# Optimization experiments

Measured on AMD Instinct MI355X. Metric: run time of the kernel, lower is better.

Reference implementation:

```python
import jax, jax.numpy as jnp
import numpy as np

NF = 64      # feature channels of h
K = 3        # dynamic filter spatial size (padding=1 in source implies k=3)
FACTOR = 4   # pixel-unshuffle factor


def shuffle_down(x, f):
    # torch pixel_unshuffle: (B,C,H*f,W*f) -> (B,C*f*f,H,W)
    B, C, H, W = x.shape
    x = x.reshape(B, C, H // f, f, W // f, f)
    x = x.transpose(0, 1, 3, 5, 2, 4)
    return x.reshape(B, C * f * f, H // f, W // f)


def _patches3x3(x):
    # x: (B,C,H,W) -> (B,C,9,H,W): zero-padded 3x3 neighborhoods, row-major taps,
    # identical to the identity-filter grouped conv (im2col) in the source.
    H, W = x.shape[-2], x.shape[-1]
    xp = jnp.pad(x, ((0, 0), (0, 0), (1, 1), (1, 1)))
    shifts = [xp[:, :, dy:dy + H, dx:dx + W] for dy in range(K) for dx in range(K)]
    return jnp.stack(shifts, axis=2)


def setup_inputs() -> dict:
    key = jax.random.key(0)
    k1, k2, k3, k4 = jax.random.split(key, 4)
    B, H, W = 2, 256, 256
    h = jax.random.normal(k1, (B, NF, H, W), dtype=jnp.float32)
    i_t = jax.random.normal(k2, (B, 3, H * FACTOR, W * FACTOR), dtype=jnp.float32)
    conv_w = jax.random.normal(k3, (K * K, 3 * FACTOR ** 2, K, K), dtype=jnp.float32) * 0.05
    conv_b = jax.random.normal(k4, (K * K,), dtype=jnp.float32) * 0.05
    return {"h": h, "i_t": i_t, "conv_w": conv_w, "conv_b": conv_b}


def reference(h, i_t, conv_w, conv_b):
    # predict per-pixel 3x3 filters from the shuffled-down guidance frame
    x = shuffle_down(i_t, FACTOR)  # (B, 48, H, W)
    f = jax.lax.conv_general_dilated(
        x, conv_w, window_strides=(1, 1), padding=((1, 1), (1, 1)),
        dimension_numbers=("NCHW", "OIHW", "NCHW"))
    filters = jax.nn.relu(f + conv_b[None, :, None, None])  # (B, 9, H, W)

    # dynamic per-pixel conv: same 3x3 filter applied to every channel of h
    patches = _patches3x3(h)  # (B, nf, 9, H, W)
    out = jnp.einsum("bcfhw,bfhw->bchw", patches, filters)  # (B, nf, H, W)
    return out
```

## Files before the change

### kernel.cpp

```cpp
#include <hip/hip_runtime.h>

#define TILE 16
#define HSZ 256
#define WSZ 256
#define NFC 64
#define PLANE (HSZ * WSZ)

typedef __attribute__((ext_vector_type(8))) short short8;
typedef __attribute__((ext_vector_type(4))) float f32x4;

__device__ inline unsigned short f2bf(float f) {
    unsigned u = __builtin_bit_cast(unsigned, f);
    return (unsigned short)((u + 0x7fffu + ((u >> 16) & 1u)) >> 16);
}

__global__ void prep_wfrag(const float* __restrict__ wbuf,
                           unsigned short* __restrict__ wfragG)
{
    const int kb   = blockIdx.x;
    const int lane = threadIdx.x;
    const int l15  = lane & 15;
    const int kg   = lane >> 4;
    unsigned short v8[8];
#pragma unroll
    for (int j = 0; j < 8; ++j) {
        const int k = kb * 32 + kg * 8 + j;
        float w = 0.f;
        if (k < 432 && l15 < 9) {
            const int kk = k / 48;
            const int ic = k - kk * 48;
            w = wbuf[l15 * 432 + ic * 9 + kk];
        }
        v8[j] = f2bf(w);
    }
    unsigned short* p = wfragG + (size_t)kb * 512 + lane * 8;
    *(ushort4*)(p)     = ushort4{v8[0], v8[1], v8[2], v8[3]};
    *(ushort4*)(p + 4) = ushort4{v8[4], v8[5], v8[6], v8[7]};
}

__global__ __launch_bounds__(256) void filter_conv_mfma3(
    const float* __restrict__ i_t,
    const unsigned short* __restrict__ wfragG,
    const float* __restrict__ bias,
    float* __restrict__ fbuf, int Bn)
{
    __shared__ __align__(16) unsigned short xs[180 * 48];

    const int tid  = threadIdx.x;
    const int X0 = blockIdx.x * 16;
    const int Y0 = blockIdx.y * 8;
    const int b  = blockIdx.z;
    const int lane = tid & 63;
    const int l15  = tid & 15;
    const int kg   = (tid >> 4) & 3;
    const int wv   = tid >> 6;

    const float bv = (l15 < 9) ? bias[l15] : 0.f;
    const float* itb = i_t + (size_t)b * 3 * (PLANE * 16);

    {
        float4 lreg[9]; int sdst[9];
#pragma unroll
        for (int k = 0; k < 9; ++k) {
            const int v = tid + 256 * k;
            const int sp = v / 12, t = v - sp * 12;
            const int c3 = t >> 2, fy = t & 3;
            const int ly = sp / 18, lx = sp - ly * 18;
            const int Y = Y0 - 1 + ly, X = X0 - 1 + lx;
            float4 val = make_float4(0.f, 0.f, 0.f, 0.f);
            if (v < 2160 && (unsigned)Y < HSZ && (unsigned)X < WSZ)
                val = *(const float4*)(itb + ((size_t)c3 * 1024 + (4 * Y + fy)) * 1024 + 4 * X);
            lreg[k] = val;
            sdst[k] = (v < 2160) ? (sp * 48 + t * 4) : -1;
        }
#pragma unroll
        for (int k = 0; k < 9; ++k) {
            if (sdst[k] >= 0) {
                ushort4 u{f2bf(lreg[k].x), f2bf(lreg[k].y), f2bf(lreg[k].z), f2bf(lreg[k].w)};
                *(ushort4*)(xs + sdst[k]) = u;
            }
        }
    }

    short8 wf[14];
#pragma unroll
    for (int kb = 0; kb < 14; ++kb)
        wf[kb] = *(const short8*)(wfragG + (size_t)kb * 512 + lane * 8);

    __syncthreads();

    f32x4 acc0 = {0.f, 0.f, 0.f, 0.f}, acc1 = acc0;
#pragma unroll
    for (int kb = 0; kb < 14; ++kb) {
        const int k0 = kb * 32 + kg * 8;
        int off = 0;
        if (k0 < 432) {
            const int kk  = k0 / 48;
            const int ic0 = k0 - kk * 48;
            const int ky  = kk / 3;
            const int kx  = kk - 3 * ky;
            off = ((2 * wv + ky) * 18 + l15 + kx) * 48 + ic0;
        }
        short8 a0 = *(const short8*)(xs + off);
        short8 a1 = *(const short8*)(xs + off + 864);
        acc0 = __builtin_amdgcn_mfma_f32_16x16x32_bf16(a0, wf[kb], acc0, 0, 0, 0);
        acc1 = __builtin_amdgcn_mfma_f32_16x16x32_bf16(a1, wf[kb], acc1, 0, 0, 0);
    }

    __syncthreads();
    float* lf = (float*)xs;
    if (l15 < 9) {
#pragma unroll
        for (int t = 0; t < 2; ++t) {
            const int py = 2 * wv + t;
            f32x4 A = t ? acc1 : acc0;
#pragma unroll
            for (int r = 0; r < 4; ++r) {
                const int px = kg * 4 + r;
                lf[l15 * 128 + py * 16 + px] = fmaxf(A[r] + bv, 0.f);
            }
        }
    }
    __syncthreads();
    {
        const int v0 = tid;
        const int oc = v0 >> 5, rem = v0 & 31, py = rem >> 2, xf4 = rem & 3;
        *(float4*)(fbuf + ((size_t)oc * Bn + b) * PLANE + (size_t)(Y0 + py) * WSZ + X0 + xf4 * 4)
            = *(const float4*)(lf + oc * 128 + py * 16 + xf4 * 4);
        if (tid < 32) {
            const int v1 = tid + 256;
            const int oc1 = v1 >> 5, rem1 = v1 & 31, py1 = rem1 >> 2, xf41 = rem1 & 3;
            *(float4*)(fbuf + ((size_t)oc1 * Bn + b) * PLANE + (size_t)(Y0 + py1) * WSZ + X0 + xf41 * 4)
                = *(const float4*)(lf + oc1 * 128 + py1 * 16 + xf41 * 4);
        }
    }
}

__global__ __launch_bounds__(256, 4) void dyn_apply5(
    const float* __restrict__ hbuf,
    const float* __restrict__ fbuf,
    float* __restrict__ out, int Bn)
{
    __shared__ __align__(16) float hs[8 * 720];

    const int tid  = threadIdx.x;
    const int pq   = tid & 7;
    const int py   = (tid >> 3) & 15;
    const int c_lo = tid >> 7;
    const int cg = blockIdx.x & 7;
    const int X0 = (blockIdx.x >> 3) * 32;
    const int Y0 = blockIdx.y * TILE;
    const int b  = blockIdx.z;

    float4 flt4[9];
    {
        const size_t pix = (size_t)b * PLANE + (size_t)(Y0 + py) * WSZ + X0 + pq * 4;
#pragma unroll
        for (int oc = 0; oc < 9; ++oc)
            flt4[oc] = *(const float4*)(fbuf + (size_t)oc * Bn * PLANE + pix);
    }

    const float* hp = hbuf + ((size_t)b * NFC + cg * 8) * PLANE;
    {
        float4 rv[6]; int dst[6];
#pragma unroll
        for (int k = 0; k < 6; ++k) {
            const int v = tid + 256 * k;
            const int c = v / 180;
            const int r = v - c * 180;
            const int row = r / 10, xq = r - row * 10;
            const int Y  = Y0 - 1 + row;
            const int X4 = X0 - 4 + xq * 4;
            float4 val = make_float4(0.f, 0.f, 0.f, 0.f);
            if (v < 1440 && (unsigned)Y < HSZ && (unsigned)X4 < WSZ)
                val = *(const float4*)(hp + (size_t)c * PLANE + (size_t)Y * WSZ + X4);
            rv[k] = val;
            dst[k] = (v < 1440) ? (c * 720 + row * 40 + xq * 4) : -1;
        }
#pragma unroll
        for (int k = 0; k < 6; ++k)
            if (dst[k] >= 0) *(float4*)(hs + dst[k]) = rv[k];
    }
    __syncthreads();

    float a[4][4];
#pragma unroll
    for (int cc = 0; cc < 4; ++cc)
#pragma unroll
        for (int j = 0; j < 4; ++j) a[cc][j] = 0.f;

#pragma unroll
    for (int cc = 0; cc < 4; ++cc) {
        const float* pl = hs + (c_lo + 2 * cc) * 720;
#pragma unroll
        for (int ky = 0; ky < 3; ++ky) {
            const float* rp = pl + (py + ky) * 40 + pq * 4;
            float4 w0 = *(const float4*)rp;
            float4 w1 = *(const float4*)(rp + 4);
            float  w8 = rp[8];
            const float vs[9] = {w0.x, w0.y, w0.z, w0.w, w1.x, w1.y, w1.z, w1.w, w8};
#pragma unroll
            for (int kx = 0; kx < 3; ++kx)
#pragma unroll
                for (int j = 0; j < 4; ++j)
                    a[cc][j] = fmaf(vs[3 + kx + j], flt4[ky * 3 + kx][j], a[cc][j]);
        }
    }

#pragma unroll
    for (int cc = 0; cc < 4; ++cc) {
        const int ch = cg * 8 + c_lo + 2 * cc;
        *(float4*)(out + ((size_t)b * NFC + ch) * PLANE
                       + (size_t)(Y0 + py) * WSZ + X0 + pq * 4)
            = make_float4(a[cc][0], a[cc][1], a[cc][2], a[cc][3]);
    }
}

__global__ __launch_bounds__(256, 2) void fused_dynfilter(
    const float* __restrict__ hbuf,
    const float* __restrict__ i_t,
    const float* __restrict__ wbuf,
    const float* __restrict__ bias,
    float* __restrict__ out)
{
    __shared__ __align__(16) float smem[15552];
    float4* xs4 = (float4*)smem;

    const int tid = threadIdx.x;
    const int px = tid & 15;
    const int py = tid >> 4;
    const int X0 = blockIdx.x * TILE;
    const int Y0 = blockIdx.y * TILE;
    const int b  = blockIdx.z;

    const float* itb = i_t + (size_t)b * 3 * 1024 * 1024;
    for (int v = tid; v < 3888; v += 256) {
        int sp = v / 12;
        int t  = v - sp * 12;
        int c3 = t >> 2, fy = t & 3;
        int ly = sp / 18, lx = sp - ly * 18;
        int Y = Y0 - 1 + ly, X = X0 - 1 + lx;
        float4 val = make_float4(0.f, 0.f, 0.f, 0.f);
        if (Y >= 0 && Y < HSZ && X >= 0 && X < WSZ)
            val = *(const float4*)(itb + ((size_t)c3 * 1024 + (4 * Y + fy)) * 1024 + 4 * X);
        xs4[t * 324 + sp] = val;
    }
    __syncthreads();

    float acc[9];
#pragma unroll
    for (int oc = 0; oc < 9; ++oc) acc[oc] = bias[oc];

#pragma unroll 1
    for (int ky = 0; ky < 3; ++ky)
#pragma unroll 1
        for (int kx = 0; kx < 3; ++kx) {
            const int sp = (py + ky) * 18 + (px + kx);
            const int kk = ky * 3 + kx;
#pragma unroll
            for (int ic4 = 0; ic4 < 12; ++ic4) {
                float4 v = xs4[ic4 * 324 + sp];
                const int chb = ((ic4 >> 2) << 4) + ((ic4 & 3) << 2);
                const float* wp = wbuf + (size_t)chb * 9 + kk;
                const float vv[4] = {v.x, v.y, v.z, v.w};
#pragma unroll
                for (int j = 0; j < 4; ++j)
#pragma unroll
                    for (int oc = 0; oc < 9; ++oc)
                        acc[oc] = fmaf(vv[j], wp[j * 9 + (size_t)oc * 432], acc[oc]);
            }
        }

    float flt[9];
#pragma unroll
    for (int oc = 0; oc < 9; ++oc) flt[oc] = fmaxf(acc[oc], 0.f);

    float4* hs4 = (float4*)smem;
#pragma unroll 1
    for (int cg = 0; cg < 16; ++cg) {
        __syncthreads();
        const float* hp = hbuf + ((size_t)b * NFC + cg * 4) * PLANE;
        for (int idx = tid; idx < 1296; idx += 256) {
            int c  = idx / 324;
            int sp = idx - c * 324;
            int ly = sp / 18, lx = sp - ly * 18;
            int Y = Y0 - 1 + ly, X = X0 - 1 + lx;
            float vv = 0.f;
            if (Y >= 0 && Y < HSZ && X >= 0 && X < WSZ)
                vv = hp[(size_t)c * PLANE + (size_t)Y * WSZ + X];
            smem[sp * 4 + c] = vv;
        }
        __syncthreads();

        float s0 = 0.f, s1 = 0.f, s2 = 0.f, s3 = 0.f;
#pragma unroll
        for (int ky = 0; ky < 3; ++ky)
#pragma unroll
            for (int kx = 0; kx < 3; ++kx) {
                float4 v = hs4[(py + ky) * 18 + (px + kx)];
                float f = flt[ky * 3 + kx];
                s0 = fmaf(v.x, f, s0);
                s1 = fmaf(v.y, f, s1);
                s2 = fmaf(v.z, f, s2);
                s3 = fmaf(v.w, f, s3);
            }
        size_t o = (((size_t)b * NFC + cg * 4) * HSZ + (Y0 + py)) * WSZ + (X0 + px);
        out[o]                     = s0;
        out[o + (size_t)PLANE]     = s1;
        out[o + (size_t)2 * PLANE] = s2;
        out[o + (size_t)3 * PLANE] = s3;
    }
}

extern "C" void kernel_launch(void* const* d_in, const int* in_sizes, int n_in,
                              void* d_out, int out_size, void* d_ws, size_t ws_size,
                              hipStream_t stream) {
    const float* h      = (const float*)d_in[0];
    const float* i_t    = (const float*)d_in[1];
    const float* conv_w = (const float*)d_in[2];
    const float* conv_b = (const float*)d_in[3];
    float* out = (float*)d_out;

    const int B = in_sizes[0] / (NFC * PLANE);
    const size_t fbuf_sz  = (size_t)9 * B * PLANE * sizeof(float);
    const size_t wfrag_sz = 14 * 512 * sizeof(unsigned short);

    if (ws_size >= fbuf_sz + wfrag_sz) {
        float* fbuf = (float*)d_ws;
        unsigned short* wfragG = (unsigned short*)((char*)d_ws + fbuf_sz);
        prep_wfrag<<<dim3(14), 64, 0, stream>>>(conv_w, wfragG);
        dim3 g1(WSZ / 16, HSZ / 8, B);
        filter_conv_mfma3<<<g1, 256, 0, stream>>>(i_t, wfragG, conv_b, fbuf, B);
        dim3 g2((WSZ / 32) * 8, HSZ / TILE, B);
        dyn_apply5<<<g2, 256, 0, stream>>>(h, fbuf, out, B);
    } else {
        dim3 grid(WSZ / TILE, HSZ / TILE, B);
        fused_dynfilter<<<grid, 256, 0, stream>>>(h, i_t, conv_w, conv_b, out);
    }
}
```

Baseline: 126.7 us.

## Fuse MFMA filter prediction and dynamic conv into one double-buffered kernel

Replaces the three-kernel pipeline (weight fragment prep, MFMA filter conv writing a global filter buffer, then dynamic apply) with a single kernel per 16x16 tile. Each block builds bf16 weight fragments in shared memory, computes its 9 filters with MFMA, keeps them in registers, and then streams the 64 h channels in groups of 8 with double-buffered shared-memory staging. This removes the global round trip of the filter buffer and two launches, and overlaps h loads with compute. In exchange, every block redoes the weight reshuffle, uses more shared memory per block, and has fewer blocks to spread across the device.

```diff
diff --git a/kernel.cpp b/kernel.cpp
--- a/kernel.cpp
+++ b/kernel.cpp
@@ -1,6 +1,5 @@
 #include <hip/hip_runtime.h>
 
-#define TILE 16
 #define HSZ 256
 #define WSZ 256
 #define NFC 64
@@ -14,301 +13,231 @@
     return (unsigned short)((u + 0x7fffu + ((u >> 16) & 1u)) >> 16);
 }
 
-__global__ void prep_wfrag(const float* __restrict__ wbuf,
-                           unsigned short* __restrict__ wfragG)
-{
-    const int kb   = blockIdx.x;
-    const int lane = threadIdx.x;
-    const int l15  = lane & 15;
-    const int kg   = lane >> 4;
-    unsigned short v8[8];
-#pragma unroll
-    for (int j = 0; j < 8; ++j) {
-        const int k = kb * 32 + kg * 8 + j;
-        float w = 0.f;
-        if (k < 432 && l15 < 9) {
-            const int kk = k / 48;
-            const int ic = k - kk * 48;
-            w = wbuf[l15 * 432 + ic * 9 + kk];
-        }
-        v8[j] = f2bf(w);
-    }
-    unsigned short* p = wfragG + (size_t)kb * 512 + lane * 8;
-    *(ushort4*)(p)     = ushort4{v8[0], v8[1], v8[2], v8[3]};
-    *(ushort4*)(p + 4) = ushort4{v8[4], v8[5], v8[6], v8[7]};
-}
-
-__global__ __launch_bounds__(256) void filter_conv_mfma3(
-    const float* __restrict__ i_t,
-    const unsigned short* __restrict__ wfragG,
-    const float* __restrict__ bias,
-    float* __restrict__ fbuf, int Bn)
-{
-    __shared__ __align__(16) unsigned short xs[180 * 48];
-
-    const int tid  = threadIdx.x;
-    const int X0 = blockIdx.x * 16;
-    const int Y0 = blockIdx.y * 8;
-    const int b  = blockIdx.z;
-    const int lane = tid & 63;
-    const int l15  = tid & 15;
-    const int kg   = (tid >> 4) & 3;
-    const int wv   = tid >> 6;
-
-    const float bv = (l15 < 9) ? bias[l15] : 0.f;
-    const float* itb = i_t + (size_t)b * 3 * (PLANE * 16);
-
-    {
-        float4 lreg[9]; int sdst[9];
-#pragma unroll
-        for (int k = 0; k < 9; ++k) {
-            const int v = tid + 256 * k;
-            const int sp = v / 12, t = v - sp * 12;
-            const int c3 = t >> 2, fy = t & 3;
-            const int ly = sp / 18, lx = sp - ly * 18;
-            const int Y = Y0 - 1 + ly, X = X0 - 1 + lx;
-            float4 val = make_float4(0.f, 0.f, 0.f, 0.f);
-            if (v < 2160 && (unsigned)Y < HSZ && (unsigned)X < WSZ)
-                val = *(const float4*)(itb + ((size_t)c3 * 1024 + (4 * Y + fy)) * 1024 + 4 * X);
-            lreg[k] = val;
-            sdst[k] = (v < 2160) ? (sp * 48 + t * 4) : -1;
-        }
-#pragma unroll
-        for (int k = 0; k < 9; ++k) {
-            if (sdst[k] >= 0) {
-                ushort4 u{f2bf(lreg[k].x), f2bf(lreg[k].y), f2bf(lreg[k].z), f2bf(lreg[k].w)};
-                *(ushort4*)(xs + sdst[k]) = u;
-            }
-        }
-    }
-
-    short8 wf[14];
-#pragma unroll
-    for (int kb = 0; kb < 14; ++kb)
-        wf[kb] = *(const short8*)(wfragG + (size_t)kb * 512 + lane * 8);
-
-    __syncthreads();
-
-    f32x4 acc0 = {0.f, 0.f, 0.f, 0.f}, acc1 = acc0;
-#pragma unroll
-    for (int kb = 0; kb < 14; ++kb) {
-        const int k0 = kb * 32 + kg * 8;
-        int off = 0;
-        if (k0 < 432) {
-            const int kk  = k0 / 48;
-            const int ic0 = k0 - kk * 48;
-            const int ky  = kk / 3;
-            const int kx  = kk - 3 * ky;
-            off = ((2 * wv + ky) * 18 + l15 + kx) * 48 + ic0;
-        }
-        short8 a0 = *(const short8*)(xs + off);
-        short8 a1 = *(const short8*)(xs + off + 864);
-        acc0 = __builtin_amdgcn_mfma_f32_16x16x32_bf16(a0, wf[kb], acc0, 0, 0, 0);
-        acc1 = __builtin_amdgcn_mfma_f32_16x16x32_bf16(a1, wf[kb], acc1, 0, 0, 0);
-    }
-
-    __syncthreads();
-    float* lf = (float*)xs;
-    if (l15 < 9) {
-#pragma unroll
-        for (int t = 0; t < 2; ++t) {
-            const int py = 2 * wv + t;
-            f32x4 A = t ? acc1 : acc0;
-#pragma unroll
-            for (int r = 0; r < 4; ++r) {
-                const int px = kg * 4 + r;
-                lf[l15 * 128 + py * 16 + px] = fmaxf(A[r] + bv, 0.f);
-            }
-        }
-    }
-    __syncthreads();
-    {
-        const int v0 = tid;
-        const int oc = v0 >> 5, rem = v0 & 31, py = rem >> 2, xf4 = rem & 3;
-        *(float4*)(fbuf + ((size_t)oc * Bn + b) * PLANE + (size_t)(Y0 + py) * WSZ + X0 + xf4 * 4)
-            = *(const float4*)(lf + oc * 128 + py * 16 + xf4 * 4);
-        if (tid < 32) {
-            const int v1 = tid + 256;
-            const int oc1 = v1 >> 5, rem1 = v1 & 31, py1 = rem1 >> 2, xf41 = rem1 & 3;
-            *(float4*)(fbuf + ((size_t)oc1 * Bn + b) * PLANE + (size_t)(Y0 + py1) * WSZ + X0 + xf41 * 4)
-                = *(const float4*)(lf + oc1 * 128 + py1 * 16 + xf41 * 4);
-        }
-    }
-}
-
-__global__ __launch_bounds__(256, 4) void dyn_apply5(
-    const float* __restrict__ hbuf,
-    const float* __restrict__ fbuf,
-    float* __restrict__ out, int Bn)
-{
-    __shared__ __align__(16) float hs[8 * 720];
-
-    const int tid  = threadIdx.x;
-    const int pq   = tid & 7;
-    const int py   = (tid >> 3) & 15;
-    const int c_lo = tid >> 7;
-    const int cg = blockIdx.x & 7;
-    const int X0 = (blockIdx.x >> 3) * 32;
-    const int Y0 = blockIdx.y * TILE;
-    const int b  = blockIdx.z;
-
-    float4 flt4[9];
-    {
-        const size_t pix = (size_t)b * PLANE + (size_t)(Y0 + py) * WSZ + X0 + pq * 4;
-#pragma unroll
-        for (int oc = 0; oc < 9; ++oc)
-            flt4[oc] = *(const float4*)(fbuf + (size_t)oc * Bn * PLANE + pix);
-    }
-
-    const float* hp = hbuf + ((size_t)b * NFC + cg * 8) * PLANE;
-    {
-        float4 rv[6]; int dst[6];
-#pragma unroll
-        for (int k = 0; k < 6; ++k) {
-            const int v = tid + 256 * k;
-            const int c = v / 180;
-            const int r = v - c * 180;
-            const int row = r / 10, xq = r - row * 10;
-            const int Y  = Y0 - 1 + row;
-            const int X4 = X0 - 4 + xq * 4;
-            float4 val = make_float4(0.f, 0.f, 0.f, 0.f);
-            if (v < 1440 && (unsigned)Y < HSZ && (unsigned)X4 < WSZ)
-                val = *(const float4*)(hp + (size_t)c * PLANE + (size_t)Y * WSZ + X4);
-            rv[k] = val;
-            dst[k] = (v < 1440) ? (c * 720 + row * 40 + xq * 4) : -1;
-        }
-#pragma unroll
-        for (int k = 0; k < 6; ++k)
-            if (dst[k] >= 0) *(float4*)(hs + dst[k]) = rv[k];
-    }
-    __syncthreads();
-
-    float a[4][4];
-#pragma unroll
-    for (int cc = 0; cc < 4; ++cc)
-#pragma unroll
-        for (int j = 0; j < 4; ++j) a[cc][j] = 0.f;
-
-#pragma unroll
-    for (int cc = 0; cc < 4; ++cc) {
-        const float* pl = hs + (c_lo + 2 * cc) * 720;
-#pragma unroll
-        for (int ky = 0; ky < 3; ++ky) {
-            const float* rp = pl + (py + ky) * 40 + pq * 4;
-            float4 w0 = *(const float4*)rp;
-            float4 w1 = *(const float4*)(rp + 4);
-            float  w8 = rp[8];
-            const float vs[9] = {w0.x, w0.y, w0.z, w0.w, w1.x, w1.y, w1.z, w1.w, w8};
-#pragma unroll
-            for (int kx = 0; kx < 3; ++kx)
-#pragma unroll
-                for (int j = 0; j < 4; ++j)
-                    a[cc][j] = fmaf(vs[3 + kx + j], flt4[ky * 3 + kx][j], a[cc][j]);
-        }
-    }
-
-#pragma unroll
-    for (int cc = 0; cc < 4; ++cc) {
-        const int ch = cg * 8 + c_lo + 2 * cc;
-        *(float4*)(out + ((size_t)b * NFC + ch) * PLANE
-                       + (size_t)(Y0 + py) * WSZ + X0 + pq * 4)
-            = make_float4(a[cc][0], a[cc][1], a[cc][2], a[cc][3]);
-    }
-}
-
-__global__ __launch_bounds__(256, 2) void fused_dynfilter(
+__global__ __launch_bounds__(256, 3) void fused_dynfilter_v2(
     const float* __restrict__ hbuf,
     const float* __restrict__ i_t,
     const float* __restrict__ wbuf,
     const float* __restrict__ bias,
     float* __restrict__ out)
 {
-    __shared__ __align__(16) float smem[15552];
-    float4* xs4 = (float4*)smem;
-
-    const int tid = threadIdx.x;
-    const int px = tid & 15;
-    const int py = tid >> 4;
-    const int X0 = blockIdx.x * TILE;
-    const int Y0 = blockIdx.y * TILE;
-    const int b  = blockIdx.z;
-
-    const float* itb = i_t + (size_t)b * 3 * 1024 * 1024;
-    for (int v = tid; v < 3888; v += 256) {
-        int sp = v / 12;
-        int t  = v - sp * 12;
-        int c3 = t >> 2, fy = t & 3;
-        int ly = sp / 18, lx = sp - ly * 18;
-        int Y = Y0 - 1 + ly, X = X0 - 1 + lx;
-        float4 val = make_float4(0.f, 0.f, 0.f, 0.f);
-        if (Y >= 0 && Y < HSZ && X >= 0 && X < WSZ)
-            val = *(const float4*)(itb + ((size_t)c3 * 1024 + (4 * Y + fy)) * 1024 + 4 * X);
-        xs4[t * 324 + sp] = val;
-    }
-    __syncthreads();
-
-    float acc[9];
-#pragma unroll
-    for (int oc = 0; oc < 9; ++oc) acc[oc] = bias[oc];
-
-#pragma unroll 1
-    for (int ky = 0; ky < 3; ++ky)
-#pragma unroll 1
-        for (int kx = 0; kx < 3; ++kx) {
-            const int sp = (py + ky) * 18 + (px + kx);
-            const int kk = ky * 3 + kx;
-#pragma unroll
-            for (int ic4 = 0; ic4 < 12; ++ic4) {
-                float4 v = xs4[ic4 * 324 + sp];
-                const int chb = ((ic4 >> 2) << 4) + ((ic4 & 3) << 2);
-                const float* wp = wbuf + (size_t)chb * 9 + kk;
-                const float vv[4] = {v.x, v.y, v.z, v.w};
-#pragma unroll
-                for (int j = 0; j < 4; ++j)
-#pragma unroll
-                    for (int oc = 0; oc < 9; ++oc)
-                        acc[oc] = fmaf(vv[j], wp[j * 9 + (size_t)oc * 432], acc[oc]);
-            }
-        }
-
-    float flt[9];
-#pragma unroll
-    for (int oc = 0; oc < 9; ++oc) flt[oc] = fmaxf(acc[oc], 0.f);
-
-    float4* hs4 = (float4*)smem;
-#pragma unroll 1
-    for (int cg = 0; cg < 16; ++cg) {
-        __syncthreads();
-        const float* hp = hbuf + ((size_t)b * NFC + cg * 4) * PLANE;
-        for (int idx = tid; idx < 1296; idx += 256) {
-            int c  = idx / 324;
-            int sp = idx - c * 324;
-            int ly = sp / 18, lx = sp - ly * 18;
-            int Y = Y0 - 1 + ly, X = X0 - 1 + lx;
-            float vv = 0.f;
-            if (Y >= 0 && Y < HSZ && X >= 0 && X < WSZ)
-                vv = hp[(size_t)c * PLANE + (size_t)Y * WSZ + X];
-            smem[sp * 4 + c] = vv;
-        }
-        __syncthreads();
-
-        float s0 = 0.f, s1 = 0.f, s2 = 0.f, s3 = 0.f;
-#pragma unroll
-        for (int ky = 0; ky < 3; ++ky)
-#pragma unroll
-            for (int kx = 0; kx < 3; ++kx) {
-                float4 v = hs4[(py + ky) * 18 + (px + kx)];
-                float f = flt[ky * 3 + kx];
-                s0 = fmaf(v.x, f, s0);
-                s1 = fmaf(v.y, f, s1);
-                s2 = fmaf(v.z, f, s2);
-                s3 = fmaf(v.w, f, s3);
-            }
-        size_t o = (((size_t)b * NFC + cg * 4) * HSZ + (Y0 + py)) * WSZ + (X0 + px);
-        out[o]                     = s0;
-        out[o + (size_t)PLANE]     = s1;
-        out[o + (size_t)2 * PLANE] = s2;
-        out[o + (size_t)3 * PLANE] = s3;
+    __shared__ __align__(16) unsigned char smem[45504];
+    unsigned short* const xs = (unsigned short*)smem;
+    unsigned short* const lw = (unsigned short*)(smem + 36288);
+    float* const lf = (float*)(smem + 36288);
+    float* const hs = (float*)smem;
+
+    const int tid  = threadIdx.x;
+    const int X0   = blockIdx.x * 16;
+    const int Y0   = blockIdx.y * 16;
+    const int b    = blockIdx.z;
+    const int lane = tid & 63;
+    const int l15  = lane & 15;
+    const int kg   = lane >> 4;
+    const int wv   = tid >> 6;
+
+    const float bv = (l15 < 9) ? bias[l15] : 0.f;
+    const float* itb = i_t + (size_t)b * 3 * (PLANE * 16);
+
+    {
+#pragma unroll
+        for (int g = 0; g < 2; ++g) {
+            float4 lreg[8]; int sdst[8];
+#pragma unroll
+            for (int k = 0; k < 8; ++k) {
+                const int v = tid + 256 * (g * 8 + k);
+                const int sp = v / 12, t = v - sp * 12;
+                const int c3 = t >> 2, fy = t & 3;
+                const int ly = sp / 18, lx = sp - ly * 18;
+                const int Y = Y0 - 1 + ly, X = X0 - 1 + lx;
+                float4 val = make_float4(0.f, 0.f, 0.f, 0.f);
+                if (v < 3888 && (unsigned)Y < HSZ && (unsigned)X < WSZ)
+                    val = *(const float4*)(itb + ((size_t)c3 * 1024 + (4 * Y + fy)) * 1024 + 4 * X);
+                lreg[k] = val;
+                sdst[k] = (v < 3888) ? (sp * 56 + t * 4) : -1;
+            }
+#pragma unroll
+            for (int k = 0; k < 8; ++k)
+                if (sdst[k] >= 0) {
+                    ushort4 u{f2bf(lreg[k].x), f2bf(lreg[k].y), f2bf(lreg[k].z), f2bf(lreg[k].w)};
+                    *(ushort4*)(xs + sdst[k]) = u;
+                }
+        }
+    }
+
+    {
+        float wreg[16]; int wdst[16];
+#pragma unroll
+        for (int k = 0; k < 16; ++k) {
+            const int v = tid + 256 * k;
+            float w = 0.f; int d = -1;
+            if (v < 3888) {
+                const int oc = v / 432, kc = v - 432 * oc;
+                const int kk = kc / 48, ic = kc - 48 * kk;
+                w = wbuf[oc * 432 + ic * 9 + kk];
+                d = kc * 9 + oc;
+            }
+            wreg[k] = w; wdst[k] = d;
+        }
+#pragma unroll
+        for (int k = 0; k < 16; ++k)
+            if (wdst[k] >= 0) lw[wdst[k]] = f2bf(wreg[k]);
+    }
+
+    __syncthreads();
+
+    short8 wf[14];
+    {
+        const int base = kg * 72 + l15;
+#pragma unroll
+        for (int kb = 0; kb < 14; ++kb) {
+            unsigned short v8[8];
+#pragma unroll
+            for (int j = 0; j < 8; ++j)
+                v8[j] = lw[base + (kb * 32 + j) * 9];
+            if (kb == 13 && kg >= 2) {
+#pragma unroll
+                for (int j = 0; j < 8; ++j) v8[j] = 0;
+            }
+            short8 w;
+#pragma unroll
+            for (int j = 0; j < 8; ++j) w[j] = (short)v8[j];
+            wf[kb] = w;
+        }
+    }
+
+    f32x4 acc[4];
+#pragma unroll
+    for (int t = 0; t < 4; ++t) acc[t] = (f32x4){0.f, 0.f, 0.f, 0.f};
+
+#pragma unroll
+    for (int kb = 0; kb < 14; ++kb) {
+        const int k0 = kb * 32 + kg * 8;
+        int off = 0;
+        if (k0 < 432) {
+            const int kk = k0 / 48, ic0 = k0 - 48 * kk;
+            const int ky = kk / 3, kx = kk - 3 * ky;
+            off = ((4 * wv + ky) * 18 + l15 + kx) * 56 + ic0;
+        }
+        const unsigned short* ap = xs + off;
+#pragma unroll
+        for (int t = 0; t < 4; ++t) {
+            short8 a = *(const short8*)(ap + t * 1008);
+            acc[t] = __builtin_amdgcn_mfma_f32_16x16x32_bf16(a, wf[kb], acc[t], 0, 0, 0);
+        }
+    }
+
+    __syncthreads();
+
+    if (l15 < 9) {
+#pragma unroll
+        for (int t = 0; t < 4; ++t) {
+            const int py = 4 * wv + t;
+#pragma unroll
+            for (int r = 0; r < 4; ++r)
+                lf[l15 * 256 + py * 16 + (kg * 4 + r)] = fmaxf(acc[t][r] + bv, 0.f);
+        }
+    }
+
+    const int pq  = tid & 3;
+    const int pyA = (tid >> 2) & 15;
+    const int clo = tid >> 6;
+
+    float4 h0reg[4]; int h0dst[4];
+    {
+        const float* hp = hbuf + (size_t)b * NFC * PLANE;
+#pragma unroll
+        for (int k = 0; k < 4; ++k) {
+            const int v = tid + 256 * k;
+            float4 val = make_float4(0.f, 0.f, 0.f, 0.f);
+            int d = -1;
+            if (v < 864) {
+                const int c = v / 108, r = v - 108 * c;
+                const int row = r / 6, xq = r - 6 * row;
+                const int Y = Y0 - 1 + row, X4 = X0 - 4 + xq * 4;
+                if ((unsigned)Y < HSZ && (unsigned)X4 < WSZ)
+                    val = *(const float4*)(hp + (size_t)c * PLANE + (size_t)Y * WSZ + X4);
+                d = c * 432 + row * 24 + xq * 4;
+            }
+            h0reg[k] = val; h0dst[k] = d;
+        }
+    }
+
+    __syncthreads();
+
+    float4 flt[9];
+#pragma unroll
+    for (int oc = 0; oc < 9; ++oc)
+        flt[oc] = *(const float4*)(lf + oc * 256 + pyA * 16 + pq * 4);
+
+#pragma unroll
+    for (int k = 0; k < 4; ++k)
+        if (h0dst[k] >= 0) *(float4*)(hs + h0dst[k]) = h0reg[k];
+
+    __syncthreads();
+
+#pragma unroll
+    for (int cg = 0; cg < 8; ++cg) {
+        const int buf = cg & 1;
+
+        float4 nreg[4]; int ndst[4];
+        if (cg < 7) {
+            const float* hp = hbuf + ((size_t)b * NFC + (cg + 1) * 8) * PLANE;
+#pragma unroll
+            for (int k = 0; k < 4; ++k) {
+                const int v = tid + 256 * k;
+                float4 val = make_float4(0.f, 0.f, 0.f, 0.f);
+                int d = -1;
+                if (v < 864) {
+                    const int c = v / 108, r = v - 108 * c;
+                    const int row = r / 6, xq = r - 6 * row;
+                    const int Y = Y0 - 1 + row, X4 = X0 - 4 + xq * 4;
+                    if ((unsigned)Y < HSZ && (unsigned)X4 < WSZ)
+                        val = *(const float4*)(hp + (size_t)c * PLANE + (size_t)Y * WSZ + X4);
+                    d = c * 432 + row * 24 + xq * 4;
+                }
+                nreg[k] = val; ndst[k] = d;
+            }
+        }
+
+        float a[2][4];
+#pragma unroll
+        for (int cc = 0; cc < 2; ++cc)
+#pragma unroll
+            for (int j = 0; j < 4; ++j) a[cc][j] = 0.f;
+
+#pragma unroll
+        for (int cc = 0; cc < 2; ++cc) {
+            const float* pl = hs + buf * 3456 + (clo * 2 + cc) * 432;
+#pragma unroll
+            for (int ky = 0; ky < 3; ++ky) {
+                const float* rp = pl + (pyA + ky) * 24 + pq * 4;
+                const float4 w0 = *(const float4*)rp;
+                const float4 w1 = *(const float4*)(rp + 4);
+                const float w8 = rp[8];
+                const float vs[9] = {w0.x, w0.y, w0.z, w0.w, w1.x, w1.y, w1.z, w1.w, w8};
+#pragma unroll
+                for (int kx = 0; kx < 3; ++kx)
+#pragma unroll
+                    for (int j = 0; j < 4; ++j)
+                        a[cc][j] = fmaf(vs[3 + kx + j], flt[ky * 3 + kx][j], a[cc][j]);
+            }
+        }
+
+#pragma unroll
+        for (int cc = 0; cc < 2; ++cc) {
+            const int ch = cg * 8 + clo * 2 + cc;
+            *(float4*)(out + ((size_t)b * NFC + ch) * PLANE
+                           + (size_t)(Y0 + pyA) * WSZ + X0 + pq * 4)
+                = make_float4(a[cc][0], a[cc][1], a[cc][2], a[cc][3]);
+        }
+
+        if (cg < 7) {
+            float* hb = hs + (buf ^ 1) * 3456;
+#pragma unroll
+            for (int k = 0; k < 4; ++k)
+                if (ndst[k] >= 0) *(float4*)(hb + ndst[k]) = nreg[k];
+            __syncthreads();
+        }
     }
 }
 
@@ -322,19 +251,6 @@
     float* out = (float*)d_out;
 
     const int B = in_sizes[0] / (NFC * PLANE);
-    const size_t fbuf_sz  = (size_t)9 * B * PLANE * sizeof(float);
-    const size_t wfrag_sz = 14 * 512 * sizeof(unsigned short);
-
-    if (ws_size >= fbuf_sz + wfrag_sz) {
-        float* fbuf = (float*)d_ws;
-        unsigned short* wfragG = (unsigned short*)((char*)d_ws + fbuf_sz);
-        prep_wfrag<<<dim3(14), 64, 0, stream>>>(conv_w, wfragG);
-        dim3 g1(WSZ / 16, HSZ / 8, B);
-        filter_conv_mfma3<<<g1, 256, 0, stream>>>(i_t, wfragG, conv_b, fbuf, B);
-        dim3 g2((WSZ / 32) * 8, HSZ / TILE, B);
-        dyn_apply5<<<g2, 256, 0, stream>>>(h, fbuf, out, B);
-    } else {
-        dim3 grid(WSZ / TILE, HSZ / TILE, B);
-        fused_dynfilter<<<grid, 256, 0, stream>>>(h, i_t, conv_w, conv_b, out);
-    }
+    dim3 grid(WSZ / 16, HSZ / 16, B);
+    fused_dynfilter_v2<<<grid, 256, 0, stream>>>(h, i_t, conv_w, conv_b, out);
 }
```

Result: no change. 125.0 us (-1.4%).
